# Kernel tuning notes

Measured on AMD Instinct MI355X. Metric: run time of the kernel, lower is better.

Reference implementation:

```python
import jax, jax.numpy as jnp
import numpy as np

C, T, B, F = 3, 100, 512, 128
HX, HZ, H, EH, L = 128, 128, 256, 128, 64


def setup_inputs() -> dict:
    key = jax.random.key(0)
    ks = jax.random.split(key, 20)
    n = lambda k, s: jax.random.normal(k, s, jnp.float32) * 0.05
    return {
        "x": jax.random.normal(ks[0], (C, T, B, F), jnp.float32),
        "phi_x_W": n(ks[1], (C, F, HX)),
        "phi_x_b": n(ks[2], (C, HX)),
        "enc_W": n(ks[3], (C, HX + H, EH)),
        "enc_b": n(ks[4], (C, EH)),
        "enc_mu_W": n(ks[5], (C, EH, L)),
        "enc_mu_b": n(ks[6], (C, L)),
        "phi_z_W": n(ks[7], (L, HZ)),
        "phi_z_b": n(ks[8], (HZ,)),
        "dec_W": n(ks[9], (C, HZ + H, EH)),
        "dec_b": n(ks[10], (C, EH)),
        "dec_mu_W": n(ks[11], (C, EH, F)),
        "dec_mu_b": n(ks[12], (C, F)),
        "rnn_Wih": n(ks[13], (HX + HZ, H)),
        "rnn_Whh": n(ks[14], (H, H)),
        "rnn_bih": n(ks[15], (H,)),
        "rnn_bhh": n(ks[16], (H,)),
        "h0": jnp.zeros((C, B, H), jnp.float32),
    }


def reference(x, phi_x_W, phi_x_b, enc_W, enc_b, enc_mu_W, enc_mu_b,
              phi_z_W, phi_z_b, dec_W, dec_b, dec_mu_W, dec_mu_b,
              rnn_Wih, rnn_Whh, rnn_bih, rnn_bhh, h0):
    # Eval-mode forward of MCRNNVAE ('long' channels): per channel, per timestep:
    # phi_x (Linear) -> encoder([phi_x, h]) -> z = mu (deterministic eval)
    # -> phi_z (Linear) -> decoder([phi_z, h]) -> RNN h update on [phi_x, phi_z].
    # NOTE: PhiBlock/VariationalBlock hidden layers have NO nonlinearity in source.
    outs = []
    for c in range(x.shape[0]):  # small fixed channel loop
        Wx, bx = phi_x_W[c], phi_x_b[c]
        We, be = enc_W[c], enc_b[c]
        Wqm, bqm = enc_mu_W[c], enc_mu_b[c]
        Wd, bd = dec_W[c], dec_b[c]
        Wpm, bpm = dec_mu_W[c], dec_mu_b[c]

        def step(h, xt):
            x_phi = xt @ Wx + bx                                    # [B,HX]
            e = jnp.concatenate([x_phi, h], axis=-1) @ We + be      # [B,EH]
            z = e @ Wqm + bqm                                       # z = qzx.loc, [B,L]
            z_phi = z @ phi_z_W + phi_z_b                           # [B,HZ]
            d = jnp.concatenate([z_phi, h], axis=-1) @ Wd + bd      # [B,EH]
            mu_p = d @ Wpm + bpm                                    # recon mean [B,F]
            rnn_in = jnp.concatenate([x_phi, z_phi], axis=-1)       # [B,HX+HZ]
            h_new = jnp.tanh(rnn_in @ rnn_Wih + rnn_bih + h @ rnn_Whh + rnn_bhh)
            return h_new, mu_p

        _, mus = jax.lax.scan(step, h0[c], x[c])  # mus: [T,B,F]
        outs.append(mus)
    return jnp.stack(outs)  # [C,T,B,F]
```

## Files before the change

### kernel.cpp

```cpp
#include <hip/hip_runtime.h>
#include <hip/hip_bf16.h>
#include <cstdint>


typedef __attribute__((ext_vector_type(8))) short short8;
typedef __attribute__((ext_vector_type(4))) float float4v;

__device__ __forceinline__ float bf2f(unsigned short u){
  union { unsigned int i; float f; } v; v.i = ((unsigned int)u) << 16; return v.f;
}
__device__ __forceinline__ unsigned short f2bf(float f){
  union { float f; unsigned int i; } v; v.f = f;
  unsigned int r = v.i + 0x7fffu + ((v.i >> 16) & 1u);
  return (unsigned short)(r >> 16);
}
__device__ __forceinline__ void st_bf2(unsigned short* p, float a, float b){
  unsigned int pa = f2bf(a), pb = f2bf(b);
  *(unsigned int*)p = pa | (pb << 16);
}
__device__ __forceinline__ float ftanh(float x){
  x = fminf(15.f, fmaxf(-15.f, x));
  float e = __expf(2.f * x);
  return (e - 1.f) * __builtin_amdgcn_rcpf(e + 1.f);
}

__device__ __forceinline__ float dotSB(const float* __restrict__ a,
                                       const float* __restrict__ b, int K, int ldb){
  float s = 0.f;
  #pragma unroll 4
  for (int k = 0; k < K; ++k) s = fmaf(a[k], b[(size_t)k * ldb], s);
  return s;
}

__global__ void pre1(const float* __restrict__ encW, const float* __restrict__ encb,
                     const float* __restrict__ Wqm, const float* __restrict__ bqm,
                     float* __restrict__ T1, float* __restrict__ T2, float* __restrict__ c0a){
  int i = blockIdx.x * 256 + threadIdx.x;
  if (i < 24576){
    int c = i >> 13, rr = (i >> 6) & 127, l = i & 63;
    T1[i] = dotSB(encW + ((size_t)c*384 + rr)*128, Wqm + (size_t)c*8192 + l, 128, 64);
  } else if (i < 73728){
    int j = i - 24576; int c = j >> 14, rr = (j >> 6) & 255, l = j & 63;
    T2[j] = dotSB(encW + ((size_t)c*384 + 128 + rr)*128, Wqm + (size_t)c*8192 + l, 128, 64);
  } else if (i < 73920){
    int j = i - 73728; int c = j >> 6, l = j & 63;
    c0a[j] = dotSB(encb + c*128, Wqm + (size_t)c*8192 + l, 128, 64) + bqm[j];
  }
}

__global__ void pre2(const float* __restrict__ T1, const float* __restrict__ T2,
                     const float* __restrict__ c0a, const float* __restrict__ Wz,
                     const float* __restrict__ bz,
                     float* __restrict__ A, float* __restrict__ Bm, float* __restrict__ c0){
  int i = blockIdx.x * 256 + threadIdx.x;
  if (i < 49152){
    int c = i >> 14, rr = (i >> 7) & 127, n = i & 127;
    A[i] = dotSB(T1 + ((size_t)c*128 + rr)*64, Wz + n, 64, 128);
  } else if (i < 147456){
    int j = i - 49152; int c = j >> 15, rr = (j >> 7) & 255, n = j & 127;
    Bm[j] = dotSB(T2 + ((size_t)c*256 + rr)*64, Wz + n, 64, 128);
  } else if (i < 147840){
    int j = i - 147456; int c = j >> 7, n = j & 127;
    c0[j] = dotSB(c0a + c*64, Wz + n, 64, 128) + bz[n];
  }
}

__global__ void pre3(const float* __restrict__ A, const float* __restrict__ Bm,
                     const float* __restrict__ c0, const float* __restrict__ Wih,
                     const float* __restrict__ Whh, const float* __restrict__ bih,
                     const float* __restrict__ bhh, const float* __restrict__ decW,
                     const float* __restrict__ decb,
                     float* __restrict__ P, float* __restrict__ Q, float* __restrict__ r,
                     float* __restrict__ D1, float* __restrict__ E1, float* __restrict__ m0a){
  int i = blockIdx.x * 256 + threadIdx.x;
  const float* Wi2 = Wih + 128*256;
  if (i < 98304){
    int c = i >> 15, rr = (i >> 8) & 127, n = i & 255;
    P[i] = Wih[rr*256 + n] + dotSB(A + ((size_t)c*128 + rr)*128, Wi2 + n, 128, 256);
  } else if (i < 294912){
    int j = i - 98304; int c = j >> 16, rr = (j >> 8) & 255, n = j & 255;
    Q[j] = Whh[rr*256 + n] + dotSB(Bm + ((size_t)c*256 + rr)*128, Wi2 + n, 128, 256);
  } else if (i < 295680){
    int j = i - 294912; int c = j >> 8, n = j & 255;
    r[j] = dotSB(c0 + c*128, Wi2 + n, 128, 256) + bih[n] + bhh[n];
  } else if (i < 344832){
    int j = i - 295680; int c = j >> 14, rr = (j >> 7) & 127, n = j & 127;
    D1[j] = dotSB(A + ((size_t)c*128 + rr)*128, decW + (size_t)c*49152 + n, 128, 128);
  } else if (i < 443136){
    int j = i - 344832; int c = j >> 15, rr = (j >> 7) & 255, n = j & 127;
    E1[j] = decW[(size_t)c*49152 + (size_t)(128 + rr)*128 + n]
          + dotSB(Bm + ((size_t)c*256 + rr)*128, decW + (size_t)c*49152 + n, 128, 128);
  } else if (i < 443520){
    int j = i - 443136; int c = j >> 7, n = j & 127;
    m0a[j] = dotSB(c0 + c*128, decW + (size_t)c*49152 + n, 128, 128) + decb[j];
  }
}

__global__ void pre4(const float* __restrict__ Wx, const float* __restrict__ bx,
                     const float* __restrict__ P, const float* __restrict__ r,
                     const float* __restrict__ D1, const float* __restrict__ E1,
                     const float* __restrict__ m0a, const float* __restrict__ Wpm,
                     const float* __restrict__ bpm,
                     float* __restrict__ R, float* __restrict__ r0,
                     float* __restrict__ M1, float* __restrict__ M2, float* __restrict__ m0){
  int i = blockIdx.x * 256 + threadIdx.x;
  if (i < 98304){
    int c = i >> 15, rr = (i >> 8) & 127, n = i & 255;
    R[i] = dotSB(Wx + ((size_t)c*128 + rr)*128, P + (size_t)c*32768 + n, 128, 256);
  } else if (i < 99072){
    int j = i - 98304; int c = j >> 8, n = j & 255;
    r0[j] = dotSB(bx + c*128, P + (size_t)c*32768 + n, 128, 256) + r[j];
  } else if (i < 148224){
    int j = i - 99072; int c = j >> 14, rr = (j >> 7) & 127, n = j & 127;
    M1[j] = dotSB(D1 + ((size_t)c*128 + rr)*128, Wpm + (size_t)c*16384 + n, 128, 128);
  } else if (i < 246528){
    int j = i - 148224; int c = j >> 15, rr = (j >> 7) & 255, n = j & 127;
    M2[j] = dotSB(E1 + ((size_t)c*256 + rr)*128, Wpm + (size_t)c*16384 + n, 128, 128);
  } else if (i < 246912){
    int j = i - 246528; int c = j >> 7, n = j & 127;
    m0[j] = dotSB(m0a + c*128, Wpm + (size_t)c*16384 + n, 128, 128) + bpm[j];
  }
}

__global__ void pre5(const float* __restrict__ Wx, const float* __restrict__ bx,
                     const float* __restrict__ M1, const float* __restrict__ m0,
                     float* __restrict__ Nn, float* __restrict__ n0){
  int i = blockIdx.x * 256 + threadIdx.x;
  if (i < 49152){
    int c = i >> 14, rr = (i >> 7) & 127, n = i & 127;
    Nn[i] = dotSB(Wx + ((size_t)c*128 + rr)*128, M1 + (size_t)c*16384 + n, 128, 128);
  } else if (i < 49536){
    int j = i - 49152; int c = j >> 7, n = j & 127;
    n0[j] = dotSB(bx + c*128, M1 + (size_t)c*16384 + n, 128, 128) + m0[j];
  }
}

#define MFMA_BF16 __builtin_amdgcn_mfma_f32_16x16x32_bf16

__global__ __launch_bounds__(512, 2)
void kernU2(const float* __restrict__ x, const float* __restrict__ Rg,
            const float* __restrict__ r0g, unsigned short* __restrict__ U){
  __shared__ unsigned short xs[128][136];
  const int m0 = blockIdx.x * 128;
  const int c  = m0 / 51200;
  const int w  = threadIdx.x >> 6;
  const int l  = threadIdx.x & 63;
  const int q  = l >> 4, m = l & 15;
  const float* __restrict__ Rc = Rg + (size_t)c * 32768;

  short8 rf[4][2];
  #pragma unroll
  for (int kt = 0; kt < 4; ++kt)
    #pragma unroll
    for (int nt = 0; nt < 2; ++nt){
      union { short8 v; unsigned short u[8]; } tmp;
      const int col = 32*w + 16*nt + m;
      #pragma unroll
      for (int j = 0; j < 8; ++j)
        tmp.u[j] = f2bf(Rc[(size_t)(32*kt + 8*q + j)*256 + col]);
      rf[kt][nt] = tmp.v;
    }
  const float r0v0 = r0g[c*256 + 32*w + m];
  const float r0v1 = r0g[c*256 + 32*w + 16 + m];

  {
    const int r  = threadIdx.x >> 2;
    const int c0 = (threadIdx.x & 3) * 32;
    const float* xr = x + (size_t)(m0 + r)*128 + c0;
    #pragma unroll
    for (int i = 0; i < 8; ++i){
      float4 v = *(const float4*)(xr + 4*i);
      st_bf2(&xs[r][c0 + 4*i],     v.x, v.y);
      st_bf2(&xs[r][c0 + 4*i + 2], v.z, v.w);
    }
  }
  __syncthreads();

  #pragma unroll 1
  for (int mt = 0; mt < 8; ++mt){
    float4v a0 = { r0v0, r0v0, r0v0, r0v0 };
    float4v a1 = { r0v1, r0v1, r0v1, r0v1 };
    #pragma unroll
    for (int kt = 0; kt < 4; ++kt){
      short8 af = *(const short8*)&xs[16*mt + m][32*kt + 8*q];
      a0 = MFMA_BF16(af, rf[kt][0], a0, 0,0,0);
      a1 = MFMA_BF16(af, rf[kt][1], a1, 0,0,0);
    }
    unsigned short* ub = U + (size_t)(m0 + 16*mt + 4*q)*256;
    ub[0*256 + 32*w + m]      = f2bf(a0.x);
    ub[1*256 + 32*w + m]      = f2bf(a0.y);
    ub[2*256 + 32*w + m]      = f2bf(a0.z);
    ub[3*256 + 32*w + m]      = f2bf(a0.w);
    ub[0*256 + 32*w + 16 + m] = f2bf(a1.x);
    ub[1*256 + 32*w + 16 + m] = f2bf(a1.y);
    ub[2*256 + 32*w + 16 + m] = f2bf(a1.z);
    ub[3*256 + 32*w + 16 + m] = f2bf(a1.w);
  }
}

__global__ __launch_bounds__(512, 2)
void kernB4(const unsigned short* __restrict__ U, const float* __restrict__ Qg,
            const float* __restrict__ h0, unsigned short* __restrict__ Hs){
  __shared__ unsigned short hHi[2][16][264];
  __shared__ unsigned short hLo[2][16][264];
  const int c  = blockIdx.x >> 5;
  const int b0 = (blockIdx.x & 31) << 4;
  const int w  = threadIdx.x >> 6;
  const int l  = threadIdx.x & 63;
  const int q  = l >> 4, m = l & 15;
  const float* __restrict__ Qc = Qg + (size_t)c * 65536;

  short8 qf[8][2];
  #pragma unroll
  for (int kt = 0; kt < 8; ++kt)
    #pragma unroll
    for (int nt = 0; nt < 2; ++nt){
      union { short8 v; unsigned short u[8]; } tmp;
      const int col = 32*w + 16*nt + m;
      #pragma unroll
      for (int j = 0; j < 8; ++j)
        tmp.u[j] = f2bf(Qc[(size_t)(32*kt + 8*q + j)*256 + col]);
      qf[kt][nt] = tmp.v;
    }

  unsigned short hiR[8];
  #pragma unroll
  for (int nt = 0; nt < 2; ++nt){
    const int col = 32*w + 16*nt + m;
    #pragma unroll
    for (int r = 0; r < 4; ++r){
      const int row = 4*q + r;
      float v = h0[((size_t)c*512 + b0 + row)*256 + col];
      unsigned short hi = f2bf(v);
      hiR[nt*4 + r] = hi;
      hHi[0][row][col] = hi;
      hLo[0][row][col] = f2bf(v - bf2f(hi));
    }
  }
  __syncthreads();

  unsigned short un[8];
  #pragma unroll
  for (int nt = 0; nt < 2; ++nt)
    #pragma unroll
    for (int r = 0; r < 4; ++r)
      un[nt*4 + r] = U[((size_t)(c*100 + 0)*512 + b0 + 4*q + r)*256 + 32*w + 16*nt + m];

  #pragma unroll 1
  for (int t = 0; t < 100; ++t){
    const int cur = t & 1, nxt = cur ^ 1;

    const size_t rowbase = (size_t)(c*100 + t)*512 + b0;
    #pragma unroll
    for (int nt = 0; nt < 2; ++nt)
      #pragma unroll
      for (int r = 0; r < 4; ++r)
        Hs[(rowbase + 4*q + r)*256 + 32*w + 16*nt + m] = hiR[nt*4 + r];

    float4v a0h = { bf2f(un[0]), bf2f(un[1]), bf2f(un[2]), bf2f(un[3]) };
    float4v a1h = { bf2f(un[4]), bf2f(un[5]), bf2f(un[6]), bf2f(un[7]) };
    float4v a0l = { 0.f, 0.f, 0.f, 0.f };
    float4v a1l = { 0.f, 0.f, 0.f, 0.f };

    const int tn = (t < 99) ? t + 1 : 99;
    unsigned short unN[8];
    #pragma unroll
    for (int nt = 0; nt < 2; ++nt)
      #pragma unroll
      for (int r = 0; r < 4; ++r)
        unN[nt*4 + r] = U[((size_t)(c*100 + tn)*512 + b0 + 4*q + r)*256 + 32*w + 16*nt + m];

    #pragma unroll
    for (int kt = 0; kt < 8; ++kt){
      short8 ahi = *(const short8*)&hHi[cur][m][32*kt + 8*q];
      short8 alo = *(const short8*)&hLo[cur][m][32*kt + 8*q];
      a0h = MFMA_BF16(ahi, qf[kt][0], a0h, 0,0,0);
      a1h = MFMA_BF16(ahi, qf[kt][1], a1h, 0,0,0);
      a0l = MFMA_BF16(alo, qf[kt][0], a0l, 0,0,0);
      a1l = MFMA_BF16(alo, qf[kt][1], a1l, 0,0,0);
    }

    float hn[8];
    hn[0] = ftanh(a0h.x + a0l.x); hn[1] = ftanh(a0h.y + a0l.y);
    hn[2] = ftanh(a0h.z + a0l.z); hn[3] = ftanh(a0h.w + a0l.w);
    hn[4] = ftanh(a1h.x + a1l.x); hn[5] = ftanh(a1h.y + a1l.y);
    hn[6] = ftanh(a1h.z + a1l.z); hn[7] = ftanh(a1h.w + a1l.w);

    #pragma unroll
    for (int nt = 0; nt < 2; ++nt){
      const int col = 32*w + 16*nt + m;
      #pragma unroll
      for (int r = 0; r < 4; ++r){
        const int row = 4*q + r;
        float v = hn[nt*4 + r];
        unsigned short hi = f2bf(v);
        hiR[nt*4 + r] = hi;
        hHi[nxt][row][col] = hi;
        hLo[nxt][row][col] = f2bf(v - bf2f(hi));
      }
    }
    #pragma unroll
    for (int i = 0; i < 8; ++i) un[i] = unN[i];

    __syncthreads();
  }
}

__global__ __launch_bounds__(512, 2)
void kernC3(const float* __restrict__ x, const unsigned short* __restrict__ Hs,
            const float* __restrict__ Nn, const float* __restrict__ M2,
            const float* __restrict__ n0, float* __restrict__ out){
  __shared__ unsigned short xs[128][136];
  const int m0 = blockIdx.x * 128;
  const int c  = m0 / 51200;
  const int w  = threadIdx.x >> 6;
  const int l  = threadIdx.x & 63;
  const int q  = l >> 4, m = l & 15;
  const int col = 16*w + m;
  const float* __restrict__ Nc  = Nn + (size_t)c * 16384;
  const float* __restrict__ M2c = M2 + (size_t)c * 32768;

  short8 bw[12];
  #pragma unroll
  for (int kt = 0; kt < 4; ++kt){
    union { short8 v; unsigned short u[8]; } tmp;
    #pragma unroll
    for (int j = 0; j < 8; ++j)
      tmp.u[j] = f2bf(Nc[(size_t)(32*kt + 8*q + j)*128 + col]);
    bw[kt] = tmp.v;
  }
  #pragma unroll
  for (int kt = 0; kt < 8; ++kt){
    union { short8 v; unsigned short u[8]; } tmp;
    #pragma unroll
    for (int j = 0; j < 8; ++j)
      tmp.u[j] = f2bf(M2c[(size_t)(32*kt + 8*q + j)*128 + col]);
    bw[4 + kt] = tmp.v;
  }
  const float nz = n0[c*128 + col];

  {
    const int r  = threadIdx.x >> 2;
    const int c0 = (threadIdx.x & 3) * 32;
    const float* xr = x + (size_t)(m0 + r)*128 + c0;
    #pragma unroll
    for (int i = 0; i < 8; ++i){
      float4 v = *(const float4*)(xr + 4*i);
      st_bf2(&xs[r][c0 + 4*i],     v.x, v.y);
      st_bf2(&xs[r][c0 + 4*i + 2], v.z, v.w);
    }
  }
  __syncthreads();

  #pragma unroll 1
  for (int mt = 0; mt < 8; ++mt){
    float4v aa = { nz, nz, nz, nz }, ab = { 0.f, 0.f, 0.f, 0.f };
    #pragma unroll
    for (int kt = 0; kt < 4; ++kt){
      short8 af = *(const short8*)&xs[16*mt + m][32*kt + 8*q];
      if (kt & 1) ab = MFMA_BF16(af, bw[kt], ab, 0,0,0);
      else        aa = MFMA_BF16(af, bw[kt], aa, 0,0,0);
    }
    const size_t mrow = (size_t)(m0 + 16*mt) + m;
    #pragma unroll
    for (int kt = 0; kt < 8; ++kt){
      short8 af = *(const short8*)&Hs[mrow*256 + 32*kt + 8*q];
      if (kt & 1) ab = MFMA_BF16(af, bw[4+kt], ab, 0,0,0);
      else        aa = MFMA_BF16(af, bw[4+kt], aa, 0,0,0);
    }
    float* ob = out + (size_t)(m0 + 16*mt + 4*q)*128 + col;
    ob[0]   = aa.x + ab.x;
    ob[128] = aa.y + ab.y;
    ob[256] = aa.z + ab.z;
    ob[384] = aa.w + ab.w;
  }
}

extern "C" void kernel_launch(void* const* d_in, const int* in_sizes, int n_in,
                              void* d_out, int out_size, void* d_ws, size_t ws_size,
                              hipStream_t stream){
  const float* x    = (const float*)d_in[0];
  const float* Wx   = (const float*)d_in[1];
  const float* bx   = (const float*)d_in[2];
  const float* encW = (const float*)d_in[3];
  const float* encb = (const float*)d_in[4];
  const float* Wqm  = (const float*)d_in[5];
  const float* bqm  = (const float*)d_in[6];
  const float* Wz   = (const float*)d_in[7];
  const float* bz   = (const float*)d_in[8];
  const float* decW = (const float*)d_in[9];
  const float* decb = (const float*)d_in[10];
  const float* Wpm  = (const float*)d_in[11];
  const float* bpm  = (const float*)d_in[12];
  const float* Wih  = (const float*)d_in[13];
  const float* Whh  = (const float*)d_in[14];
  const float* bih  = (const float*)d_in[15];
  const float* bhh  = (const float*)d_in[16];
  const float* h0   = (const float*)d_in[17];

  float* ws = (float*)d_ws;
  size_t off = 0;
  auto alloc = [&](size_t n){ float* p = ws + off; off += n; return p; };
  float* T1  = alloc(24576);  float* T2  = alloc(49152);  float* c0a = alloc(192);
  float* A   = alloc(49152);  float* Bm  = alloc(98304);  float* c0  = alloc(384);
  float* P   = alloc(98304);  float* Q   = alloc(196608); float* r   = alloc(768);
  float* D1  = alloc(49152);  float* E1  = alloc(98304);  float* m0a = alloc(384);
  float* R   = alloc(98304);  float* r0  = alloc(768);
  float* M1  = alloc(49152);  float* M2  = alloc(98304);  float* m0  = alloc(384);
  float* Nn  = alloc(49152);  float* n0  = alloc(384);
  unsigned short* Hs = (unsigned short*)(ws + off); off += 19660800;
  unsigned short* U  = (unsigned short*)d_out;

  hipLaunchKernelGGL(pre1, dim3(289),  dim3(256), 0, stream, encW, encb, Wqm, bqm, T1, T2, c0a);
  hipLaunchKernelGGL(pre2, dim3(578),  dim3(256), 0, stream, T1, T2, c0a, Wz, bz, A, Bm, c0);
  hipLaunchKernelGGL(pre3, dim3(1733), dim3(256), 0, stream, A, Bm, c0, Wih, Whh, bih, bhh,
                     decW, decb, P, Q, r, D1, E1, m0a);
  hipLaunchKernelGGL(pre4, dim3(965),  dim3(256), 0, stream, Wx, bx, P, r, D1, E1, m0a,
                     Wpm, bpm, R, r0, M1, M2, m0);
  hipLaunchKernelGGL(pre5, dim3(194),  dim3(256), 0, stream, Wx, bx, M1, m0, Nn, n0);
  hipLaunchKernelGGL(kernU2, dim3(1200), dim3(512), 0, stream, x, R, r0, U);
  hipLaunchKernelGGL(kernB4, dim3(96),   dim3(512), 0, stream, U, Q, h0, Hs);
  hipLaunchKernelGGL(kernC3, dim3(1200), dim3(512), 0, stream, x, Hs, Nn, M2, n0, (float*)d_out);
}
```

Baseline: 476.6 us.

## Transpose U layout for vector loads and pack hi/lo hidden state in LDS

New measurement: 761.9 us. 59.9% more time.

```diff
diff --git a/kernel.cpp b/kernel.cpp
--- a/kernel.cpp
+++ b/kernel.cpp
@@ -4,6 +4,7 @@
 
 
 typedef __attribute__((ext_vector_type(8))) short short8;
+typedef __attribute__((ext_vector_type(4))) short short4v;
 typedef __attribute__((ext_vector_type(4))) float float4v;
 
 __device__ __forceinline__ float bf2f(unsigned short u){
@@ -176,6 +177,9 @@
   }
   __syncthreads();
 
+  const size_t ct = (size_t)(m0 >> 9);
+  const int bbase = (m0 & 511);
+
   #pragma unroll 1
   for (int mt = 0; mt < 8; ++mt){
     float4v a0 = { r0v0, r0v0, r0v0, r0v0 };
@@ -186,23 +190,21 @@
       a0 = MFMA_BF16(af, rf[kt][0], a0, 0,0,0);
       a1 = MFMA_BF16(af, rf[kt][1], a1, 0,0,0);
     }
-    unsigned short* ub = U + (size_t)(m0 + 16*mt + 4*q)*256;
-    ub[0*256 + 32*w + m]      = f2bf(a0.x);
-    ub[1*256 + 32*w + m]      = f2bf(a0.y);
-    ub[2*256 + 32*w + m]      = f2bf(a0.z);
-    ub[3*256 + 32*w + m]      = f2bf(a0.w);
-    ub[0*256 + 32*w + 16 + m] = f2bf(a1.x);
-    ub[1*256 + 32*w + 16 + m] = f2bf(a1.y);
-    ub[2*256 + 32*w + 16 + m] = f2bf(a1.z);
-    ub[3*256 + 32*w + 16 + m] = f2bf(a1.w);
+    const int b = bbase + 16*mt + 4*q;
+    short4v s0, s1;
+    s0[0] = (short)f2bf(a0.x); s0[1] = (short)f2bf(a0.y);
+    s0[2] = (short)f2bf(a0.z); s0[3] = (short)f2bf(a0.w);
+    s1[0] = (short)f2bf(a1.x); s1[1] = (short)f2bf(a1.y);
+    s1[2] = (short)f2bf(a1.z); s1[3] = (short)f2bf(a1.w);
+    *(short4v*)(U + (ct*256 + 32*w + m)*512 + b)      = s0;
+    *(short4v*)(U + (ct*256 + 32*w + 16 + m)*512 + b) = s1;
   }
 }
 
 __global__ __launch_bounds__(512, 2)
-void kernB4(const unsigned short* __restrict__ U, const float* __restrict__ Qg,
+void kernB5(const unsigned short* __restrict__ U, const float* __restrict__ Qg,
             const float* __restrict__ h0, unsigned short* __restrict__ Hs){
-  __shared__ unsigned short hHi[2][16][264];
-  __shared__ unsigned short hLo[2][16][264];
+  __shared__ unsigned int hI[2][16][257];
   const int c  = blockIdx.x >> 5;
   const int b0 = (blockIdx.x & 31) << 4;
   const int w  = threadIdx.x >> 6;
@@ -233,18 +235,15 @@
       float v = h0[((size_t)c*512 + b0 + row)*256 + col];
       unsigned short hi = f2bf(v);
       hiR[nt*4 + r] = hi;
-      hHi[0][row][col] = hi;
-      hLo[0][row][col] = f2bf(v - bf2f(hi));
+      hI[0][row][col] = (unsigned int)hi | ((unsigned int)f2bf(v - bf2f(hi)) << 16);
     }
   }
   __syncthreads();
 
-  unsigned short un[8];
-  #pragma unroll
-  for (int nt = 0; nt < 2; ++nt)
-    #pragma unroll
-    for (int r = 0; r < 4; ++r)
-      un[nt*4 + r] = U[((size_t)(c*100 + 0)*512 + b0 + 4*q + r)*256 + 32*w + 16*nt + m];
+  const unsigned short* Ub0 = U + ((size_t)(c*100)*256 + 32*w + m)*512 + b0 + 4*q;
+  const unsigned short* Ub1 = U + ((size_t)(c*100)*256 + 32*w + 16 + m)*512 + b0 + 4*q;
+  short4v un0 = *(const short4v*)Ub0;
+  short4v un1 = *(const short4v*)Ub1;
 
   #pragma unroll 1
   for (int t = 0; t < 100; ++t){
@@ -257,27 +256,35 @@
       for (int r = 0; r < 4; ++r)
         Hs[(rowbase + 4*q + r)*256 + 32*w + 16*nt + m] = hiR[nt*4 + r];
 
-    float4v a0h = { bf2f(un[0]), bf2f(un[1]), bf2f(un[2]), bf2f(un[3]) };
-    float4v a1h = { bf2f(un[4]), bf2f(un[5]), bf2f(un[6]), bf2f(un[7]) };
+    float4v a0h = { bf2f((unsigned short)un0[0]), bf2f((unsigned short)un0[1]),
+                    bf2f((unsigned short)un0[2]), bf2f((unsigned short)un0[3]) };
+    float4v a1h = { bf2f((unsigned short)un1[0]), bf2f((unsigned short)un1[1]),
+                    bf2f((unsigned short)un1[2]), bf2f((unsigned short)un1[3]) };
     float4v a0l = { 0.f, 0.f, 0.f, 0.f };
     float4v a1l = { 0.f, 0.f, 0.f, 0.f };
 
     const int tn = (t < 99) ? t + 1 : 99;
-    unsigned short unN[8];
-    #pragma unroll
-    for (int nt = 0; nt < 2; ++nt)
-      #pragma unroll
-      for (int r = 0; r < 4; ++r)
-        unN[nt*4 + r] = U[((size_t)(c*100 + tn)*512 + b0 + 4*q + r)*256 + 32*w + 16*nt + m];
-
+    short4v unN0 = *(const short4v*)(Ub0 + (size_t)tn*131072);
+    short4v unN1 = *(const short4v*)(Ub1 + (size_t)tn*131072);
+
+    const unsigned int* hrow = &hI[cur][m][0];
     #pragma unroll
     for (int kt = 0; kt < 8; ++kt){
-      short8 ahi = *(const short8*)&hHi[cur][m][32*kt + 8*q];
-      short8 alo = *(const short8*)&hLo[cur][m][32*kt + 8*q];
-      a0h = MFMA_BF16(ahi, qf[kt][0], a0h, 0,0,0);
-      a1h = MFMA_BF16(ahi, qf[kt][1], a1h, 0,0,0);
-      a0l = MFMA_BF16(alo, qf[kt][0], a0l, 0,0,0);
-      a1l = MFMA_BF16(alo, qf[kt][1], a1l, 0,0,0);
+      uint4 u0 = *(const uint4*)(hrow + 32*kt + 8*q);
+      uint4 u1 = *(const uint4*)(hrow + 32*kt + 8*q + 4);
+      union { short8 v; unsigned int d[4]; } ahi, alo;
+      ahi.d[0] = __builtin_amdgcn_perm(u0.y, u0.x, 0x05040100u);
+      ahi.d[1] = __builtin_amdgcn_perm(u0.w, u0.z, 0x05040100u);
+      ahi.d[2] = __builtin_amdgcn_perm(u1.y, u1.x, 0x05040100u);
+      ahi.d[3] = __builtin_amdgcn_perm(u1.w, u1.z, 0x05040100u);
+      alo.d[0] = __builtin_amdgcn_perm(u0.y, u0.x, 0x07060302u);
+      alo.d[1] = __builtin_amdgcn_perm(u0.w, u0.z, 0x07060302u);
+      alo.d[2] = __builtin_amdgcn_perm(u1.y, u1.x, 0x07060302u);
+      alo.d[3] = __builtin_amdgcn_perm(u1.w, u1.z, 0x07060302u);
+      a0h = MFMA_BF16(ahi.v, qf[kt][0], a0h, 0,0,0);
+      a1h = MFMA_BF16(ahi.v, qf[kt][1], a1h, 0,0,0);
+      a0l = MFMA_BF16(alo.v, qf[kt][0], a0l, 0,0,0);
+      a1l = MFMA_BF16(alo.v, qf[kt][1], a1l, 0,0,0);
     }
 
     float hn[8];
@@ -295,12 +302,10 @@
         float v = hn[nt*4 + r];
         unsigned short hi = f2bf(v);
         hiR[nt*4 + r] = hi;
-        hHi[nxt][row][col] = hi;
-        hLo[nxt][row][col] = f2bf(v - bf2f(hi));
+        hI[nxt][row][col] = (unsigned int)hi | ((unsigned int)f2bf(v - bf2f(hi)) << 16);
       }
     }
-    #pragma unroll
-    for (int i = 0; i < 8; ++i) un[i] = unN[i];
+    un0 = unN0; un1 = unN1;
 
     __syncthreads();
   }
@@ -419,6 +424,6 @@
                      Wpm, bpm, R, r0, M1, M2, m0);
   hipLaunchKernelGGL(pre5, dim3(194),  dim3(256), 0, stream, Wx, bx, M1, m0, Nn, n0);
   hipLaunchKernelGGL(kernU2, dim3(1200), dim3(512), 0, stream, x, R, r0, U);
-  hipLaunchKernelGGL(kernB4, dim3(96),   dim3(512), 0, stream, U, Q, h0, Hs);
+  hipLaunchKernelGGL(kernB5, dim3(96),   dim3(512), 0, stream, U, Q, h0, Hs);
   hipLaunchKernelGGL(kernC3, dim3(1200), dim3(512), 0, stream, x, Hs, Nn, M2, n0, (float*)d_out);
 }
```
